# Performance work log

Measured on AMD Instinct MI355X. Metric: run time of the kernel, lower is better.

Reference implementation:

```python
import jax, jax.numpy as jnp
import numpy as np

B = 50000        # mini-batch nodes
NB, M, D = 4, 256, 32   # branches, codebook size, per-branch dim
C = NB * D       # in_channels = out_channels = 128
E = 1000000      # edges per block (intra and cross)
N_GLOBAL = 100000


def setup_inputs() -> dict:
    key = jax.random.key(0)
    ks = jax.random.split(key, 16)
    return {
        "X_B": jax.random.normal(ks[0], (B, C), dtype=jnp.float32),
        "edge_src_bb": jax.random.randint(ks[1], (E,), 0, B),
        "edge_dst_bb": jax.random.randint(ks[2], (E,), 0, B),
        "edge_w_bb": jax.random.uniform(ks[3], (E,), dtype=jnp.float32),
        "edge_src_bm": jax.random.randint(ks[4], (E,), 0, N_GLOBAL),
        "edge_dst_bm": jax.random.randint(ks[5], (E,), 0, B),
        "edge_w_bm": jax.random.uniform(ks[6], (E,), dtype=jnp.float32),
        "c_indices": jax.random.randint(ks[7], (N_GLOBAL,), 0, M),
        "warm_up_rate": jnp.ones((1,), dtype=jnp.float32),
        "codebook": jax.random.normal(ks[8], (NB, M, D), dtype=jnp.float32),
        "vq_grad": jax.random.normal(ks[9], (NB, M, D), dtype=jnp.float32) * 0.01,
        "W_conv": jax.random.normal(ks[10], (NB, D, D), dtype=jnp.float32) / np.sqrt(D),
        "b_conv": jax.random.normal(ks[11], (NB, D), dtype=jnp.float32) * 0.01,
        "W_fc": jax.random.normal(ks[12], (C, C), dtype=jnp.float32) / np.sqrt(C),
        "b_fc": jax.random.normal(ks[13], (C,), dtype=jnp.float32) * 0.01,
    }


def reference(X_B, edge_src_bb, edge_dst_bb, edge_w_bb, edge_src_bm, edge_dst_bm,
              edge_w_bm, c_indices, warm_up_rate, codebook, vq_grad,
              W_conv, b_conv, W_fc, b_fc):
    wr = warm_up_rate[0]
    # split features into NB branches: [NB, B, D]
    Xb = X_B.reshape(B, NB, D).transpose(1, 0, 2)
    # X_input = cat([X_B, codebook * warm_up_rate]) per branch -> [NB, B+M, D]
    X_in = jnp.concatenate([Xb, codebook * wr], axis=1)
    # GCNConv (normalize=False): linear transform then edge-weighted aggregation
    h = jnp.einsum('nbd,nde->nbe', X_in, W_conv)
    # mapper: remap out-of-batch endpoints of cross edges to codeword rows
    src_bm = B + c_indices[edge_src_bm]          # [E] indices into codeword rows
    out = jnp.zeros_like(h)
    # A_BB block: intra-batch message passing
    out = out.at[:, edge_dst_bb].add(edge_w_bb[None, :, None] * h[:, edge_src_bb])
    # A_BM block: batch nodes receive from codewords (quantized neighbors)
    out = out.at[:, edge_dst_bm].add(edge_w_bm[None, :, None] * h[:, src_bm])
    # A_MB block: codeword rows receive from batch nodes (for info_backward)
    out = out.at[:, src_bm].add(edge_w_bm[None, :, None] * h[:, edge_dst_bm])
    out = out + b_conv[:, None, :]
    # info_backward routes approximated gradient through codeword outputs
    info_backward = jnp.sum(out[:, B:] * vq_grad) * wr
    # concat branch outputs for batch nodes, second fc, skip connection
    Xcat = out[:, :B].transpose(1, 0, 2).reshape(B, C)
    Y = Xcat @ W_fc + b_fc + X_B
    return (Y, info_backward)
```

## Files before the change

### kernel.cpp

```cpp
#include <hip/hip_runtime.h>
#include <hip/hip_bf16.h>

#define BN    50000
#define NBR   4
#define MM    256
#define DD    32
#define CC    128
#define EE    1000000
#define ROWS  (BN + MM)
#define NEDGE (2 * EE)
#define SCAN_BLOCKS 49
#define REDB  196

template <int ISBF> struct IO;

template <> struct IO<0> {
    static __device__ float ld(const void* p, long i) { return ((const float*)p)[i]; }
    static __device__ float2 ld2(const void* p, long i) {
        const float* f = (const float*)p + i;
        return make_float2(f[0], f[1]);
    }
    static __device__ void st(void* p, long i, float v) { ((float*)p)[i] = v; }
    static __device__ void st2(void* p, long i, float2 v) {
        float* f = (float*)p + i; f[0] = v.x; f[1] = v.y;
    }
};

template <> struct IO<1> {
    static __device__ float b2f(unsigned short u) {
        return __uint_as_float(((unsigned)u) << 16);
    }
    static __device__ unsigned short f2b(float f) {
        unsigned x = __float_as_uint(f);
        unsigned r = x + 0x7fffu + ((x >> 16) & 1u);
        return (unsigned short)(r >> 16);
    }
    static __device__ float ld(const void* p, long i) {
        return b2f(((const unsigned short*)p)[i]);
    }
    static __device__ float2 ld2(const void* p, long i) {
        unsigned v = *(const unsigned*)((const unsigned short*)p + i);
        return make_float2(b2f((unsigned short)(v & 0xffffu)),
                           b2f((unsigned short)(v >> 16)));
    }
    static __device__ void st(void* p, long i, float v) {
        ((unsigned short*)p)[i] = f2b(v);
    }
    static __device__ void st2(void* p, long i, float2 v) {
        unsigned o = ((unsigned)f2b(v.x)) | (((unsigned)f2b(v.y)) << 16);
        *(unsigned*)((unsigned short*)p + i) = o;
    }
};

template <int ISBF> struct HIO;
template <> struct HIO<0> {
    static __device__ float2 ld(const float* h, long row, int l) {
        return *(const float2*)(h + row * CC + 2 * l);
    }
    static __device__ void st(float* h, long row, int l, float2 v) {
        *(float2*)(h + row * CC + 2 * l) = v;
    }
};
template <> struct HIO<1> {
    static __device__ float2 ld(const float* h, long row, int l) {
        unsigned u = ((const unsigned*)h)[row * (CC / 2) + l];
        return make_float2(IO<1>::b2f((unsigned short)(u & 0xffffu)),
                           IO<1>::b2f((unsigned short)(u >> 16)));
    }
    static __device__ void st(float* h, long row, int l, float2 v) {
        unsigned o = ((unsigned)IO<1>::f2b(v.x)) | (((unsigned)IO<1>::f2b(v.y)) << 16);
        ((unsigned*)h)[row * (CC / 2) + l] = o;
    }
};

static __device__ inline void unpack8(int4 v, float* f) {
    unsigned a = (unsigned)v.x, b = (unsigned)v.y, c = (unsigned)v.z, d = (unsigned)v.w;
    f[0] = IO<1>::b2f((unsigned short)(a & 0xffffu)); f[1] = IO<1>::b2f((unsigned short)(a >> 16));
    f[2] = IO<1>::b2f((unsigned short)(b & 0xffffu)); f[3] = IO<1>::b2f((unsigned short)(b >> 16));
    f[4] = IO<1>::b2f((unsigned short)(c & 0xffffu)); f[5] = IO<1>::b2f((unsigned short)(c >> 16));
    f[6] = IO<1>::b2f((unsigned short)(d & 0xffffu)); f[7] = IO<1>::b2f((unsigned short)(d >> 16));
}
static __device__ inline void fma8(float* acc, float w, int4 v) {
    float f[8]; unpack8(v, f);
#pragma unroll
    for (int k = 0; k < 8; k++) acc[k] += w * f[k];
}
static __device__ inline float dot8(const float* hi, int4 v) {
    float f[8]; unpack8(v, f);
    float s = 0.f;
#pragma unroll
    for (int k = 0; k < 8; k++) s += hi[k] * f[k];
    return s;
}

__global__ void kDetect(const void* warm, int* flag) {
    flag[0] = (((const unsigned short*)warm)[0] == 0x3F80u) ? 1 : 0;
}

template <int ISBF>
__device__ void kA_body(const void* X_B, const void* codebook, const void* W_conv,
                        const void* warm, float* __restrict__ hout,
                        float* __restrict__ hcw, float* sW, float* sX) {
    int tid = threadIdx.x;
    int w = tid >> 6, l = tid & 63;
    for (int k = tid; k < NBR * DD * DD; k += 256)
        sW[k] = IO<ISBF>::ld(W_conv, k);
    int r = blockIdx.x * 4 + w;
    int c0 = 2 * l, n = c0 >> 5, e = c0 & 31;
    float2 x2;
    if (r < BN) {
        x2 = IO<ISBF>::ld2(X_B, (long)r * CC + c0);
    } else {
        int m = r - BN;
        float wr = IO<ISBF>::ld(warm, 0);
        x2 = IO<ISBF>::ld2(codebook, (long)n * MM * DD + m * DD + e);
        x2.x *= wr; x2.y *= wr;
    }
    sX[w * CC + c0] = x2.x;
    sX[w * CC + c0 + 1] = x2.y;
    __syncthreads();
    float2 acc = make_float2(0.f, 0.f);
#pragma unroll
    for (int d = 0; d < DD; d++) {
        float xv = sX[w * CC + n * DD + d];
        float2 wv = *(const float2*)&sW[n * DD * DD + d * DD + e];
        acc.x += xv * wv.x;
        acc.y += xv * wv.y;
    }
    if (r < BN) HIO<ISBF>::st(hout, r, l, acc);
    else        HIO<ISBF>::st(hcw, r - BN, l, acc);
}
__global__ __launch_bounds__(256) void kA(const int* flag, const void* X_B,
                                          const void* codebook, const void* W_conv,
                                          const void* warm, float* hout, float* hcw) {
    __shared__ float sW[NBR * DD * DD];
    __shared__ float sX[4 * CC];
    if (*flag) kA_body<1>(X_B, codebook, W_conv, warm, hout, hcw, sW, sX);
    else       kA_body<0>(X_B, codebook, W_conv, warm, hout, hcw, sW, sX);
}

__global__ void kHist(const int* __restrict__ edst_bb, const int* __restrict__ edst_bm,
                      int* __restrict__ counts) {
    long stride = (long)gridDim.x * blockDim.x;
    for (long i = (long)blockIdx.x * blockDim.x + threadIdx.x; i < NEDGE; i += stride) {
        int dst = (i < EE) ? edst_bb[i] : edst_bm[i - EE];
        atomicAdd(&counts[dst], 1);
    }
}

__global__ __launch_bounds__(1024) void kScan1(const int* __restrict__ counts,
                                               int* __restrict__ offsets,
                                               int* __restrict__ tileSum) {
    __shared__ int s[1024];
    int tid = threadIdx.x;
    int i = blockIdx.x * 1024 + tid;
    int v = (i < BN) ? counts[i] : 0;
    s[tid] = v;
    __syncthreads();
    for (int off = 1; off < 1024; off <<= 1) {
        int x = (tid >= off) ? s[tid - off] : 0;
        __syncthreads();
        s[tid] += x;
        __syncthreads();
    }
    if (i < BN) offsets[i] = s[tid] - v;
    if (tid == 1023) tileSum[blockIdx.x] = s[tid];
}
__global__ void kScan2(int* tileSum) {
    int run = 0;
    for (int t = 0; t < SCAN_BLOCKS; t++) {
        int v = tileSum[t];
        tileSum[t] = run;
        run += v;
    }
}
__global__ __launch_bounds__(1024) void kScan3(int* __restrict__ offsets,
                                               const int* __restrict__ tileSum,
                                               int* __restrict__ cursor) {
    int i = blockIdx.x * 1024 + threadIdx.x;
    if (i < BN) {
        int o = offsets[i] + tileSum[blockIdx.x];
        offsets[i] = o;
        cursor[i] = o;
    }
}

template <int ISBF>
__device__ void kFill_body(const int* esrc_bb, const int* edst_bb, const void* ew_bb,
                           const int* esrc_bm, const int* edst_bm, const void* ew_bm,
                           const int* c_idx, int* cursor, int2* entries) {
    long stride = (long)gridDim.x * blockDim.x;
    for (long i = (long)blockIdx.x * blockDim.x + threadIdx.x; i < NEDGE; i += stride) {
        int src, dst; float w;
        if (i < EE) {
            src = esrc_bb[i]; dst = edst_bb[i]; w = IO<ISBF>::ld(ew_bb, i);
        } else {
            long j = i - EE;
            src = BN + c_idx[esrc_bm[j]]; dst = edst_bm[j]; w = IO<ISBF>::ld(ew_bm, j);
        }
        int pos = atomicAdd(&cursor[dst], 1);
        entries[pos] = make_int2(src, __float_as_int(w));
    }
}
__global__ void kFill(const int* flag, const int* esrc_bb, const int* edst_bb,
                      const void* ew_bb, const int* esrc_bm, const int* edst_bm,
                      const void* ew_bm, const int* c_idx, int* cursor, int2* entries) {
    if (*flag) kFill_body<1>(esrc_bb, edst_bb, ew_bb, esrc_bm, edst_bm, ew_bm, c_idx, cursor, entries);
    else       kFill_body<0>(esrc_bb, edst_bb, ew_bb, esrc_bm, edst_bm, ew_bm, c_idx, cursor, entries);
}

__device__ void kGS_bf(int slice,
                       const unsigned short* __restrict__ hbatch,
                       const unsigned short* __restrict__ hcw,
                       const int2* __restrict__ entries,
                       const int* __restrict__ offsets, const int* __restrict__ counts,
                       const void* b_conv, const void* vq_grad, void* t,
                       float* __restrict__ infoP) {
    int tid = threadIdx.x;
    int l = tid & 63;
    int g = l >> 2;
    int q = l & 3;
    int n = slice;
    int e0 = q * 8;
    int c0 = n * 32 + e0;
    const unsigned short* gb = (const unsigned short*)vq_grad + (long)n * MM * DD + e0;
    float bc[8];
    unpack8(*(const int4*)((const unsigned short*)b_conv + n * DD + e0), bc);

    int wid = (int)((blockIdx.x * blockDim.x + tid) >> 6);
    int nw  = (int)((gridDim.x * blockDim.x) >> 6);

    for (int i = wid; i < BN; i += nw) {
        int start = __builtin_amdgcn_readfirstlane(offsets[i]);
        int deg   = __builtin_amdgcn_readfirstlane(counts[i]);
        const long* ep = (const long*)(entries + start);

        float hi[8];
        unpack8(*(const int4*)(hbatch + (long)i * CC + c0), hi);
        float acc[8] = {0.f, 0.f, 0.f, 0.f, 0.f, 0.f, 0.f, 0.f};
        float info = 0.f;

        for (int j = 0; j < deg; j += 64) {
            int src[4]; float wj[4];
#pragma unroll
            for (int u = 0; u < 4; u++) {
                int idx = j + 16 * u + g;
                long e8 = __builtin_nontemporal_load(ep + (idx < deg ? idx : deg - 1));
                src[u] = (int)(unsigned)(e8 & 0xffffffffL);
                wj[u]  = (idx < deg) ? __int_as_float((int)(e8 >> 32)) : 0.f;
            }
#pragma unroll
            for (int u = 0; u < 4; u++) {
                int4 hv;
                if (src[u] < BN) {
                    hv = *(const int4*)(hbatch + (long)src[u] * CC + c0);
                } else {
                    hv = *(const int4*)(hcw + (long)(src[u] - BN) * CC + c0);
                    if (wj[u] != 0.f) {
                        int4 gv = *(const int4*)(gb + (long)(src[u] - BN) * DD);
                        info += wj[u] * dot8(hi, gv);
                    }
                }
                fma8(acc, wj[u], hv);
            }
        }
#pragma unroll
        for (int k = 0; k < 8; k++) {
            acc[k] += __shfl_xor(acc[k], 4);
            acc[k] += __shfl_xor(acc[k], 8);
            acc[k] += __shfl_xor(acc[k], 16);
            acc[k] += __shfl_xor(acc[k], 32);
        }
        for (int off = 32; off; off >>= 1) info += __shfl_xor(info, off);
        if (l == 0) infoP[(long)slice * BN + i] = info;
        if (g == 0) {
            unsigned o[4];
#pragma unroll
            for (int d = 0; d < 4; d++)
                o[d] = ((unsigned)IO<1>::f2b(acc[2 * d] + bc[2 * d])) |
                       (((unsigned)IO<1>::f2b(acc[2 * d + 1] + bc[2 * d + 1])) << 16);
            *(int4*)((unsigned short*)t + (long)i * CC + c0) = make_int4(o[0], o[1], o[2], o[3]);
        }
    }
}

__device__ void kG_body_f32(const float* __restrict__ hbatch, const float* __restrict__ hcw,
                            const int2* __restrict__ entries,
                            const int* __restrict__ offsets, const int* __restrict__ counts,
                            const void* b_conv, const void* vq_grad, void* t,
                            float* __restrict__ infoP) {
    int tid = threadIdx.x;
    int l = tid & 63;
    int c0 = 2 * l, n = c0 >> 5, e = c0 & 31;
    int wid = (int)((blockIdx.x * blockDim.x + tid) >> 6);
    int nw  = (int)((gridDim.x * blockDim.x) >> 6);
    for (int i = wid; i < BN; i += nw) {
        int start = __builtin_amdgcn_readfirstlane(offsets[i]);
        int deg   = __builtin_amdgcn_readfirstlane(counts[i]);
        const int2* ep = entries + start;
        float2 hi = HIO<0>::ld(hbatch, i, l);
        long gbase = (long)n * MM * DD + e;
        float2 acc = make_float2(0.f, 0.f);
        float info = 0.f;
        for (int j = 0; j < deg; j++) {
            int2 ev = ep[j];
            float wj = __int_as_float(ev.y);
            const float* src = (ev.x < BN) ? (hbatch + (long)ev.x * CC)
                                           : (hcw + (long)(ev.x - BN) * CC);
            float2 hv = *(const float2*)(src + c0);
            acc.x += wj * hv.x;
            acc.y += wj * hv.y;
            if (ev.x >= BN) {
                float2 gv = IO<0>::ld2(vq_grad, gbase + (long)(ev.x - BN) * DD);
                info += wj * (hi.x * gv.x + hi.y * gv.y);
            }
        }
        float2 b2 = IO<0>::ld2(b_conv, n * DD + e);
        IO<0>::st2(t, (long)i * CC + c0, make_float2(acc.x + b2.x, acc.y + b2.y));
        for (int off = 32; off; off >>= 1) info += __shfl_xor(info, off);
        if (l == 0) infoP[i] = info;
    }
}
__global__ __launch_bounds__(256, 8) void kGatherS(const int* flag, int slice,
                                                   const float* hout, const float* hcw,
                                                   const int2* entries,
                                                   const int* offsets, const int* counts,
                                                   const void* b_conv, const void* vq_grad,
                                                   void* t, float* infoP) {
    if (*flag) kGS_bf(slice, (const unsigned short*)hout, (const unsigned short*)hcw,
                      entries, offsets, counts, b_conv, vq_grad, t, infoP);
    else if (slice == 0)
        kG_body_f32(hout, hcw, entries, offsets, counts, b_conv, vq_grad, t, infoP);
}

__global__ __launch_bounds__(1024) void kRed(const float* __restrict__ infoP, float* ibAcc) {
    __shared__ float s[1024];
    int tid = threadIdx.x;
    long i = (long)blockIdx.x * 1024 + tid;
    s[tid] = (i < 4L * BN) ? infoP[i] : 0.f;
    __syncthreads();
    for (int st = 512; st; st >>= 1) {
        if (tid < st) s[tid] += s[tid + st];
        __syncthreads();
    }
    if (tid == 0) atomicAdd(ibAcc, s[0]);
}

template <int ISBF>
__device__ void kFC_body(const void* t, const void* W_fc, const void* b_fc,
                         const void* X_B, void* Y, float* sT, float* sW) {
    int tid = threadIdx.x;
    int w = tid >> 6, l = tid & 63;
    int c0 = 2 * l;
    int r0 = blockIdx.x * 32;
    for (int k = tid; k < 32 * CC / 2; k += 512) {
        int row = k >> 6, c = (k & 63) * 2;
        float2 v = make_float2(0.f, 0.f);
        if (r0 + row < BN) v = IO<ISBF>::ld2(t, (long)(r0 + row) * CC + c);
        sT[row * CC + c] = v.x;
        sT[row * CC + c + 1] = v.y;
    }
    float2 y[4];
#pragma unroll
    for (int rr = 0; rr < 4; rr++) y[rr] = make_float2(0.f, 0.f);
    for (int ch = 0; ch < 4; ch++) {
        __syncthreads();
        for (int k = tid; k < 32 * CC / 2; k += 512) {
            int cc = k >> 6, c = (k & 63) * 2;
            float2 v = IO<ISBF>::ld2(W_fc, (long)(ch * 32 + cc) * CC + c);
            sW[cc * CC + c] = v.x;
            sW[cc * CC + c + 1] = v.y;
        }
        __syncthreads();
#pragma unroll 8
        for (int cc = 0; cc < 32; cc++) {
            float2 wv = *(const float2*)&sW[cc * CC + c0];
#pragma unroll
            for (int rr = 0; rr < 4; rr++) {
                float tv = sT[(w * 4 + rr) * CC + ch * 32 + cc];
                y[rr].x += tv * wv.x;
                y[rr].y += tv * wv.y;
            }
        }
    }
    float2 bf = IO<ISBF>::ld2(b_fc, c0);
#pragma unroll
    for (int rr = 0; rr < 4; rr++) {
        int r = r0 + w * 4 + rr;
        if (r < BN) {
            float2 xb = IO<ISBF>::ld2(X_B, (long)r * CC + c0);
            IO<ISBF>::st2(Y, (long)r * CC + c0,
                          make_float2(y[rr].x + bf.x + xb.x, y[rr].y + bf.y + xb.y));
        }
    }
}
__global__ __launch_bounds__(512) void kFC(const int* flag, const void* t, const void* W_fc,
                                           const void* b_fc, const void* X_B, void* Y) {
    __shared__ float sT[32 * CC];
    __shared__ float sW[32 * CC];
    if (*flag) kFC_body<1>(t, W_fc, b_fc, X_B, Y, sT, sW);
    else       kFC_body<0>(t, W_fc, b_fc, X_B, Y, sT, sW);
}

template <int ISBF>
__device__ void kF_body(const void* b_conv, const void* vq_grad, const void* warm,
                        const float* ibAcc, void* out, float* sred) {
    int tid = threadIdx.x;
    float a = 0.f;
    for (int idx = tid; idx < NBR * MM * DD; idx += 256) {
        int nn = idx >> 13, dd = idx & 31;
        a += IO<ISBF>::ld(b_conv, nn * DD + dd) * IO<ISBF>::ld(vq_grad, idx);
    }
    sred[tid] = a;
    __syncthreads();
    for (int s = 128; s; s >>= 1) {
        if (tid < s) sred[tid] += sred[tid + s];
        __syncthreads();
    }
    if (tid == 0) {
        float wr = IO<ISBF>::ld(warm, 0);
        IO<ISBF>::st(out, (long)BN * CC, wr * (ibAcc[0] + sred[0]));
    }
}
__global__ __launch_bounds__(256) void kFinal(const int* flag, const void* b_conv,
                                              const void* vq_grad, const void* warm,
                                              const float* ibAcc, void* out) {
    __shared__ float sred[256];
    if (*flag) kF_body<1>(b_conv, vq_grad, warm, ibAcc, out, sred);
    else       kF_body<0>(b_conv, vq_grad, warm, ibAcc, out, sred);
}

extern "C" void kernel_launch(void* const* d_in, const int* in_sizes, int n_in,
                              void* d_out, int out_size, void* d_ws, size_t ws_size,
                              hipStream_t stream) {
    (void)in_sizes; (void)n_in; (void)out_size;
    const void* X_B      = d_in[0];
    const int*  esrc_bb  = (const int*)d_in[1];
    const int*  edst_bb  = (const int*)d_in[2];
    const void* ew_bb    = d_in[3];
    const int*  esrc_bm  = (const int*)d_in[4];
    const int*  edst_bm  = (const int*)d_in[5];
    const void* ew_bm    = d_in[6];
    const int*  c_idx    = (const int*)d_in[7];
    const void* warm     = d_in[8];
    const void* codebook = d_in[9];
    const void* vq_grad  = d_in[10];
    const void* W_conv   = d_in[11];
    const void* b_conv   = d_in[12];
    const void* W_fc     = d_in[13];
    const void* b_fc     = d_in[14];

    char* ws = (char*)d_ws;
    float* hcw     = (float*)ws;  ws += (size_t)MM * CC * 4;
    float* tbuf    = (float*)ws;  ws += (size_t)BN * CC * 4;
    int2*  entries = (int2*)ws;   ws += (size_t)NEDGE * 8;
    int*   counts  = (int*)ws;    ws += (size_t)BN * 4;
    int*   offsets = (int*)ws;    ws += (size_t)BN * 4;
    int*   cursor  = (int*)ws;    ws += (size_t)BN * 4;
    float* infoP   = (float*)ws;  ws += (size_t)4 * BN * 4;
    int*   tileSum = (int*)ws;    ws += 64 * 4;
    float* ibAcc   = (float*)ws;  ws += 16;
    int*   flag    = (int*)ws;    ws += 16;
    if ((size_t)(ws - (char*)d_ws) > ws_size) return;

    float* hout = (float*)d_out;

    hipMemsetAsync(counts, 0, (size_t)BN * 4, stream);
    hipMemsetAsync(ibAcc, 0, 4, stream);
    hipMemsetAsync(infoP, 0, (size_t)4 * BN * 4, stream);
    kDetect<<<1, 1, 0, stream>>>(warm, flag);
    kA<<<ROWS / 4, 256, 0, stream>>>(flag, X_B, codebook, W_conv, warm, hout, hcw);
    kHist<<<1024, 256, 0, stream>>>(edst_bb, edst_bm, counts);
    kScan1<<<SCAN_BLOCKS, 1024, 0, stream>>>(counts, offsets, tileSum);
    kScan2<<<1, 1, 0, stream>>>(tileSum);
    kScan3<<<SCAN_BLOCKS, 1024, 0, stream>>>(offsets, tileSum, cursor);
    kFill<<<1024, 256, 0, stream>>>(flag, esrc_bb, edst_bb, ew_bb, esrc_bm, edst_bm,
                                    ew_bm, c_idx, cursor, entries);
    for (int slice = 0; slice < 4; slice++)
        kGatherS<<<2048, 256, 0, stream>>>(flag, slice, hout, hcw, entries, offsets,
                                           counts, b_conv, vq_grad, tbuf, infoP);
    kRed<<<REDB, 1024, 0, stream>>>(infoP, ibAcc);
    kFC<<<(BN + 31) / 32, 512, 0, stream>>>(flag, tbuf, W_fc, b_fc, X_B, d_out);
    kFinal<<<1, 256, 0, stream>>>(flag, b_conv, vq_grad, warm, ibAcc, d_out);
}
```

Baseline: 642.0 us.

## Store bf16 conv features branch-major and use nontemporal output stores

The bf16 path of the transform kernel now writes h in a per-branch layout ([NB][rows][32]) instead of row-major [rows][128]. The per-slice gather kernel then reads contiguous 64-byte rows from a slice, so that slice's working set (about 3.2 MB per branch) is denser and more cache-friendly during random gathers. The aggregated output is also written with nontemporal stores to avoid polluting the cache. If other kernels still read h in the old row-major layout, results could be wrong.

```diff
diff --git a/kernel.cpp b/kernel.cpp
--- a/kernel.cpp
+++ b/kernel.cpp
@@ -61,17 +61,6 @@
         *(float2*)(h + row * CC + 2 * l) = v;
     }
 };
-template <> struct HIO<1> {
-    static __device__ float2 ld(const float* h, long row, int l) {
-        unsigned u = ((const unsigned*)h)[row * (CC / 2) + l];
-        return make_float2(IO<1>::b2f((unsigned short)(u & 0xffffu)),
-                           IO<1>::b2f((unsigned short)(u >> 16)));
-    }
-    static __device__ void st(float* h, long row, int l, float2 v) {
-        unsigned o = ((unsigned)IO<1>::f2b(v.x)) | (((unsigned)IO<1>::f2b(v.y)) << 16);
-        ((unsigned*)h)[row * (CC / 2) + l] = o;
-    }
-};
 
 static __device__ inline void unpack8(int4 v, float* f) {
     unsigned a = (unsigned)v.x, b = (unsigned)v.y, c = (unsigned)v.z, d = (unsigned)v.w;
@@ -91,6 +80,13 @@
 #pragma unroll
     for (int k = 0; k < 8; k++) s += hi[k] * f[k];
     return s;
+}
+
+typedef int iv4 __attribute__((ext_vector_type(4)));
+static __device__ inline void nt_store16(void* p, unsigned a, unsigned b,
+                                         unsigned c, unsigned d) {
+    iv4 x; x[0] = (int)a; x[1] = (int)b; x[2] = (int)c; x[3] = (int)d;
+    __builtin_nontemporal_store(x, (iv4*)p);
 }
 
 __global__ void kDetect(const void* warm, int* flag) {
@@ -127,8 +123,14 @@
         acc.x += xv * wv.x;
         acc.y += xv * wv.y;
     }
-    if (r < BN) HIO<ISBF>::st(hout, r, l, acc);
-    else        HIO<ISBF>::st(hcw, r - BN, l, acc);
+    if (ISBF) {
+        unsigned o = ((unsigned)IO<1>::f2b(acc.x)) | (((unsigned)IO<1>::f2b(acc.y)) << 16);
+        if (r < BN) ((unsigned*)hout)[((long)n * BN + r) * 16 + (l & 15)] = o;
+        else        ((unsigned*)hcw)[((long)n * MM + (r - BN)) * 16 + (l & 15)] = o;
+    } else {
+        if (r < BN) HIO<0>::st(hout, r, l, acc);
+        else        HIO<0>::st(hcw, r - BN, l, acc);
+    }
 }
 __global__ __launch_bounds__(256) void kA(const int* flag, const void* X_B,
                                           const void* codebook, const void* W_conv,
@@ -210,7 +212,7 @@
 }
 
 __device__ void kGS_bf(int slice,
-                       const unsigned short* __restrict__ hbatch,
+                       const unsigned short* __restrict__ hs,
                        const unsigned short* __restrict__ hcw,
                        const int2* __restrict__ entries,
                        const int* __restrict__ offsets, const int* __restrict__ counts,
@@ -223,6 +225,8 @@
     int n = slice;
     int e0 = q * 8;
     int c0 = n * 32 + e0;
+    const unsigned short* hsl  = hs  + (long)n * BN * 32;
+    const unsigned short* hcwl = hcw + (long)n * MM * 32;
     const unsigned short* gb = (const unsigned short*)vq_grad + (long)n * MM * DD + e0;
     float bc[8];
     unpack8(*(const int4*)((const unsigned short*)b_conv + n * DD + e0), bc);
@@ -236,7 +240,7 @@
         const long* ep = (const long*)(entries + start);
 
         float hi[8];
-        unpack8(*(const int4*)(hbatch + (long)i * CC + c0), hi);
+        unpack8(*(const int4*)(hsl + (long)i * 32 + e0), hi);
         float acc[8] = {0.f, 0.f, 0.f, 0.f, 0.f, 0.f, 0.f, 0.f};
         float info = 0.f;
 
@@ -253,9 +257,9 @@
             for (int u = 0; u < 4; u++) {
                 int4 hv;
                 if (src[u] < BN) {
-                    hv = *(const int4*)(hbatch + (long)src[u] * CC + c0);
+                    hv = *(const int4*)(hsl + (long)src[u] * 32 + e0);
                 } else {
-                    hv = *(const int4*)(hcw + (long)(src[u] - BN) * CC + c0);
+                    hv = *(const int4*)(hcwl + (long)(src[u] - BN) * 32 + e0);
                     if (wj[u] != 0.f) {
                         int4 gv = *(const int4*)(gb + (long)(src[u] - BN) * DD);
                         info += wj[u] * dot8(hi, gv);
@@ -279,7 +283,7 @@
             for (int d = 0; d < 4; d++)
                 o[d] = ((unsigned)IO<1>::f2b(acc[2 * d] + bc[2 * d])) |
                        (((unsigned)IO<1>::f2b(acc[2 * d + 1] + bc[2 * d + 1])) << 16);
-            *(int4*)((unsigned short*)t + (long)i * CC + c0) = make_int4(o[0], o[1], o[2], o[3]);
+            nt_store16((unsigned short*)t + (long)i * CC + c0, o[0], o[1], o[2], o[3]);
         }
     }
 }
```

New measurement: 629.9 us. Within noise of the previous version (-1.9%).
